# Kernel optimization log

Hardware: AMD Instinct MI355X
Metric: run time of the kernel (lower is better)

## Reference

```python
import jax, jax.numpy as jnp
import numpy as np

DIM = 192
NUM_HEADS = 6
WIN = (8, 8)
N = WIN[0] * WIN[1]  # 64 tokens per window


def _relative_position_index():
    ch = np.arange(WIN[0]); cw = np.arange(WIN[1])
    coords = np.stack(np.meshgrid(ch, cw, indexing='ij'))          # (2, Wh, Ww)
    flat = coords.reshape(2, -1)                                    # (2, N)
    rel = flat[:, :, None] - flat[:, None, :]                       # (2, N, N)
    rel = rel.transpose(1, 2, 0).copy()                             # (N, N, 2)
    rel[..., 0] += WIN[0] - 1
    rel[..., 1] += WIN[1] - 1
    rel[..., 0] *= 2 * WIN[1] - 1
    return jnp.asarray(rel.sum(-1), dtype=jnp.int32)                # (N, N)

RPI = _relative_position_index()


def setup_inputs() -> dict:
    key = jax.random.key(0)
    ks = jax.random.split(key, 20)
    B_, T, M, C = 128, 4, 4, DIM
    nW = 64
    x = jax.random.normal(ks[0], (B_, T, N, C), dtype=jnp.float32)
    x_kv = jax.random.normal(ks[1], (B_, M, N, C), dtype=jnp.float32)
    u = jax.random.uniform(ks[2], (nW, N, N))
    mask = jnp.where(u > 0.9, jnp.float32(-100.0), jnp.float32(0.0))
    s = 0.02
    p = lambda k, shape: jax.random.normal(k, shape, dtype=jnp.float32) * s
    return {
        'x': x, 'x_kv': x_kv, 'mask': mask,
        'rpb_table': p(ks[3], ((2 * WIN[0] - 1) * (2 * WIN[1] - 1), NUM_HEADS)),
        'q_w': p(ks[4], (C, C)), 'q_b': jnp.zeros((C,), jnp.float32),
        'kv_w': p(ks[5], (2 * C, C)), 'kv_b': jnp.zeros((2 * C,), jnp.float32),
        'pos_emb': jax.random.normal(ks[6], (N, C), dtype=jnp.float32) / C ** 0.5,
        'pq_w': p(ks[7], (C, C)), 'pq_b': jnp.zeros((C,), jnp.float32),
        'pk_w': p(ks[8], (C, C)), 'pk_b': jnp.zeros((C,), jnp.float32),
        'pv_w': p(ks[9], (C, C)), 'pv_b': jnp.zeros((C,), jnp.float32),
        'po_w': p(ks[10], (C, C)), 'po_b': jnp.zeros((C,), jnp.float32),
        'proj_w': p(ks[11], (C, C)), 'proj_b': jnp.zeros((C,), jnp.float32),
    }


def reference(x, x_kv, mask, rpb_table, q_w, q_b, kv_w, kv_b, pos_emb,
              pq_w, pq_b, pk_w, pk_b, pv_w, pv_b, po_w, po_b, proj_w, proj_b):
    B_, T, _, C = x.shape
    M = x_kv.shape[1]
    nH = NUM_HEADS
    hd = C // nH
    scale = hd ** -0.5

    # projections -> (B_, T, nH, N, hd) and (B_, M, nH, N, hd)
    q = (x @ q_w.T + q_b).reshape(B_, T, N, nH, hd).transpose(0, 1, 3, 2, 4)
    kv = (x_kv @ kv_w.T + kv_b).reshape(B_, M, N, 2, nH, hd)
    k = kv[:, :, :, 0].transpose(0, 1, 3, 2, 4)
    v = kv[:, :, :, 1].transpose(0, 1, 3, 2, 4)

    # scores: (B_, T, M, nH, N, N)
    attn = jnp.einsum('bthnd,bmhed->btmhne', q * scale, k)

    # relative position bias gather
    rpb = rpb_table[RPI.reshape(-1)].reshape(N, N, nH).transpose(2, 0, 1)
    attn = attn + rpb[None, None, None]

    # shifted-window mask (per window index within B_ = b * nW)
    nW = mask.shape[0]
    b = B_ // nW
    attn = attn.reshape(b, nW, T, M, nH, N, N) + mask[None, :, None, None, None]
    attn = attn.reshape(B_, T, M, nH, N, N)

    attn = jax.nn.softmax(attn, axis=-1)
    out = jnp.einsum('btmhne,bmhed->btmhnd', attn, v)
    # faithful to torch: transpose(1,2) then reshape (B_, T, M, N, C)
    out = jnp.swapaxes(out, 1, 2).reshape(B_, T, M, N, C)
    xp = out.reshape(B_ * T, M, N, C)

    # AttentionPooling1d over the M reference axis
    avg = xp.mean(axis=1, keepdims=True)
    xp = jnp.concatenate([avg, xp], axis=1) + pos_emb[None, None]   # (BT, M+1, N, C)
    BT = xp.shape[0]
    seq = xp.transpose(1, 2, 0, 3).reshape((M + 1) * N, BT, C)      # (m n) b c
    qq = (seq[:N] @ pq_w.T + pq_b).reshape(N, BT, nH, hd)
    kk = (seq @ pk_w.T + pk_b).reshape(-1, BT, nH, hd)
    vv = (seq @ pv_w.T + pv_b).reshape(-1, BT, nH, hd)
    a = jnp.einsum('qbhd,kbhd->bhqk', qq * scale, kk)
    a = jax.nn.softmax(a, axis=-1)
    o = jnp.einsum('bhqk,kbhd->qbhd', a, vv).reshape(N, BT, C)
    o = o @ po_w.T + po_b                                           # (N, BT, C)
    o = o.transpose(1, 0, 2).reshape(B_, T, N, C)

    o = jax.nn.gelu(o, approximate=False)
    return o @ proj_w.T + proj_b
```

## Files before the change

kernel.cpp:

```cpp
#include <hip/hip_runtime.h>
#include <math.h>


typedef float f32x4 __attribute__((ext_vector_type(4)));
typedef short s16x8 __attribute__((ext_vector_type(8)));
typedef unsigned short u16x4 __attribute__((ext_vector_type(4)));
typedef unsigned short u16x8 __attribute__((ext_vector_type(8)));

__device__ __forceinline__ unsigned short f2bf(float f) {
    union { float f; unsigned u; } c; c.f = f;
    return (unsigned short)((c.u + 0x7fffu + ((c.u >> 16) & 1u)) >> 16);
}
__device__ __forceinline__ float bf2f(unsigned short h) {
    union { unsigned u; float f; } c; c.u = ((unsigned)h) << 16;
    return c.f;
}

__global__ void wcvt_kernel(const float* __restrict__ q_w, const float* __restrict__ kv_w,
                            const float* __restrict__ pq_w, const float* __restrict__ pk_w,
                            const float* __restrict__ pv_w, const float* __restrict__ po_w,
                            const float* __restrict__ proj_w, unsigned short* __restrict__ wbf)
{
    int i = blockIdx.x * 256 + threadIdx.x;
    if (i >= 294912) return;
    const float* src; int off;
    if      (i < 36864)  { src = q_w;    off = 0; }
    else if (i < 110592) { src = kv_w;   off = 36864; }
    else if (i < 147456) { src = pq_w;   off = 110592; }
    else if (i < 184320) { src = pk_w;   off = 147456; }
    else if (i < 221184) { src = pv_w;   off = 184320; }
    else if (i < 258048) { src = po_w;   off = 221184; }
    else                 { src = proj_w; off = 258048; }
    wbf[i] = f2bf(src[i - off]);
}

__global__ void prep_kernel(unsigned short* __restrict__ xp, const float* __restrict__ pos,
                            unsigned short* __restrict__ t0b)
{
    int i = blockIdx.x * 256 + threadIdx.x;
    int c8 = (i % 24) * 8;
    int n  = (i / 24) & 63;
    int bt = i / (24 * 64);
    float4 p0 = *reinterpret_cast<const float4*>(&pos[n * 192 + c8]);
    float4 p1 = *reinterpret_cast<const float4*>(&pos[n * 192 + c8 + 4]);
    float pv[8] = {p0.x, p0.y, p0.z, p0.w, p1.x, p1.y, p1.z, p1.w};
    float acc[8] = {0, 0, 0, 0, 0, 0, 0, 0};
    size_t base = (size_t)bt * 49152 + n * 192 + c8;
#pragma unroll
    for (int m = 0; m < 4; m++) {
        u16x8 v = *reinterpret_cast<const u16x8*>(&xp[base + m * 12288]);
        u16x8 o;
#pragma unroll
        for (int e = 0; e < 8; e++) {
            float f = bf2f(v[e]) + pv[e];
            acc[e] += f;
            o[e] = f2bf(f);
        }
        *reinterpret_cast<u16x8*>(&xp[base + m * 12288]) = o;
    }
    u16x8 t;
#pragma unroll
    for (int e = 0; e < 8; e++) t[e] = f2bf(acc[e] * 0.25f);
    *reinterpret_cast<u16x8*>(&t0b[(size_t)(bt * 64 + n) * 192 + c8]) = t;
}

template <int SRC, int EPI, int OUTBF>
__global__ __launch_bounds__(256, 3)
void mgemm_kernel(const float* __restrict__ A, const unsigned short* __restrict__ Ab,
                  const unsigned short* __restrict__ Ab2,
                  const unsigned short* __restrict__ W0, const unsigned short* __restrict__ W1,
                  const float* __restrict__ b0, const float* __restrict__ b1,
                  void* __restrict__ C0v, void* __restrict__ C1v, int c0)
{
    __shared__ __align__(16) char As[128 * 192];
    __shared__ __align__(16) char Bs[96 * 192];
    const int tid = threadIdx.x;
    const int gm0 = blockIdx.x * 128;
    const int gn0 = blockIdx.y * 96;
    const int wid = tid >> 6;
    const int wm = wid >> 1, wn = wid & 1;
    const int lane = tid & 63;
    const int lr = lane & 15;
    const int lk = lane >> 4;

    const bool hiN = (gn0 >= 192);
    const unsigned short* Wsel = (EPI == 3 && hiN) ? W1 : W0;
    const int wrow0 = (EPI == 3 && hiN) ? (gn0 - 192) : gn0;

    f32x4 acc[4][3];
#pragma unroll
    for (int i = 0; i < 4; i++)
#pragma unroll
        for (int j = 0; j < 3; j++) acc[i][j] = (f32x4){0.f, 0.f, 0.f, 0.f};

    for (int kb = 0; kb < 192; kb += 96) {
        if (SRC == 0) {
#pragma unroll
            for (int it = 0; it < 12; it++) {
                int f4 = tid + it * 256;
                int row = f4 / 24;
                int kc4 = (f4 - row * 24) * 4;
                float4 v = *reinterpret_cast<const float4*>(
                    &A[(size_t)(gm0 + row) * 192 + kb + kc4]);
                u16x4 bvv;
                bvv[0] = f2bf(v.x); bvv[1] = f2bf(v.y);
                bvv[2] = f2bf(v.z); bvv[3] = f2bf(v.w);
                int boff = (kc4 * 2) ^ ((row & 3) << 4);
                *reinterpret_cast<u16x4*>(As + row * 192 + boff) = bvv;
            }
        } else {
#pragma unroll
            for (int it = 0; it < 6; it++) {
                int f8 = tid + it * 256;
                int row = f8 / 12;
                int c16 = f8 - row * 12;
                const unsigned short* src;
                if (SRC == 3) {
                    src = &Ab[(size_t)(gm0 + row) * 192 + kb + c16 * 8];
                } else {
                    int g = gm0 + row;
                    int bt = g / 320, tok = g - bt * 320; bt += c0;
                    src = (tok < 64)
                        ? &Ab2[(size_t)(bt * 64 + tok) * 192 + kb + c16 * 8]
                        : &Ab[(size_t)bt * 49152 + ((tok >> 6) - 1) * 12288
                              + (tok & 63) * 192 + kb + c16 * 8];
                }
                u16x8 v = *reinterpret_cast<const u16x8*>(src);
                int boff = (c16 * 16) ^ ((row & 3) << 4);
                *reinterpret_cast<u16x8*>(As + row * 192 + boff) = v;
            }
        }
        for (int f8 = tid; f8 < 1152; f8 += 256) {
            int row = f8 / 12;
            int c16 = f8 - row * 12;
            u16x8 v = *reinterpret_cast<const u16x8*>(
                &Wsel[(size_t)(wrow0 + row) * 192 + kb + c16 * 8]);
            int boff = (c16 * 16) ^ ((row & 3) << 4);
            *reinterpret_cast<u16x8*>(Bs + row * 192 + boff) = v;
        }
        __syncthreads();

#pragma unroll
        for (int ks = 0; ks < 3; ks++) {
            s16x8 af[4], bf[3];
#pragma unroll
            for (int i = 0; i < 4; i++) {
                int row = wm * 64 + i * 16 + lr;
                int off = (ks * 64 + lk * 16) ^ ((row & 3) << 4);
                af[i] = *reinterpret_cast<const s16x8*>(As + row * 192 + off);
            }
#pragma unroll
            for (int j = 0; j < 3; j++) {
                int row = wn * 48 + j * 16 + lr;
                int off = (ks * 64 + lk * 16) ^ ((row & 3) << 4);
                bf[j] = *reinterpret_cast<const s16x8*>(Bs + row * 192 + off);
            }
#pragma unroll
            for (int i = 0; i < 4; i++)
#pragma unroll
                for (int j = 0; j < 3; j++)
                    acc[i][j] = __builtin_amdgcn_mfma_f32_16x16x32_bf16(
                        af[i], bf[j], acc[i][j], 0, 0, 0);
        }
        __syncthreads();
    }

#pragma unroll
    for (int j = 0; j < 3; j++) {
        int bcol = gn0 + wn * 48 + j * 16 + lr;
        float bv = (EPI == 3 && bcol >= 192) ? b1[bcol - 192] : b0[bcol];
        void* dst = C0v;
        int oc = bcol;
        if ((EPI == 2 || EPI == 3) && bcol >= 192) { dst = C1v; oc = bcol - 192; }
#pragma unroll
        for (int i = 0; i < 4; i++) {
            int rbase = gm0 + wm * 64 + i * 16 + lk * 4;
#pragma unroll
            for (int r = 0; r < 4; r++) {
                float v = acc[i][j][r] + bv;
                if (EPI == 1) v = 0.5f * v * (1.f + erff(v * 0.70710678118654752440f));
                size_t idx = (size_t)(rbase + r) * 192 + oc;
                if (OUTBF) ((unsigned short*)dst)[idx] = f2bf(v);
                else       ((float*)dst)[idx] = v;
            }
        }
    }
}

__global__ __launch_bounds__(768, 1)
void winattn_kernel(const float* __restrict__ qbuf,
                    const unsigned short* __restrict__ kbuf,
                    const unsigned short* __restrict__ vbuf,
                    const float* __restrict__ mask,
                    const float* __restrict__ rpbt, unsigned short* __restrict__ xp)
{
    __shared__ float klds[64 * 192];
    __shared__ float vlds[64 * 192];
    __shared__ float mlds[64 * 65];
    __shared__ float rldsT[6 * 225];
    __shared__ float exm[768];
    __shared__ float exl[768];
    __shared__ unsigned obuf[6 * 64 * 17];
    const int tid = threadIdx.x;
    const int bid = blockIdx.x;
    const int bb = bid >> 4;
    const int t = (bid >> 2) & 3;
    const int m = bid & 3;
    const int w = tid >> 6;
    const int h = w >> 1;
    const int lane = tid & 63;

    const int kvbase = (bb * 4 + m) * 12288;
#pragma unroll
    for (int it = 0; it < 2; it++) {
        int i8 = tid + it * 768;
        u16x8 kq = *reinterpret_cast<const u16x8*>(&kbuf[kvbase + i8 * 8]);
        u16x8 vq = *reinterpret_cast<const u16x8*>(&vbuf[kvbase + i8 * 8]);
        f32x4 k0, k1, v0, v1;
#pragma unroll
        for (int e = 0; e < 4; e++) {
            k0[e] = bf2f(kq[e]); k1[e] = bf2f(kq[e + 4]);
            v0[e] = bf2f(vq[e]); v1[e] = bf2f(vq[e + 4]);
        }
        *reinterpret_cast<f32x4*>(&klds[i8 * 8]) = k0;
        *reinterpret_cast<f32x4*>(&klds[i8 * 8 + 4]) = k1;
        *reinterpret_cast<f32x4*>(&vlds[i8 * 8]) = v0;
        *reinterpret_cast<f32x4*>(&vlds[i8 * 8 + 4]) = v1;
    }
    const int widx = bb & 63;
    for (int f = tid; f < 4096; f += 768)
        mlds[(f >> 6) * 65 + (f & 63)] = mask[widx * 4096 + f];
    for (int f = tid; f < 1350; f += 768) {
        int hh = f / 225, rr = f - hh * 225;
        rldsT[f] = rpbt[rr * 6 + hh];
    }

    float qreg[32];
    const int qbase = ((bb * 4 + t) * 64 + lane) * 192 + h * 32;
#pragma unroll
    for (int j = 0; j < 8; j++) {
        float4 v = *reinterpret_cast<const float4*>(&qbuf[qbase + j * 4]);
        qreg[4 * j] = v.x; qreg[4 * j + 1] = v.y;
        qreg[4 * j + 2] = v.z; qreg[4 * j + 3] = v.w;
    }
    __syncthreads();

    const float scale = 0.17677669529663688110f;
    const int ni = lane >> 3, nj = lane & 7;
    const int e0 = (w & 1) << 5;
    float s[32];
#pragma unroll
    for (int ee = 0; ee < 32; ee++) {
        int e = e0 + ee;
        const float4* kr = reinterpret_cast<const float4*>(&klds[e * 192 + h * 32]);
        float d0 = 0, d1 = 0, d2 = 0, d3 = 0;
#pragma unroll
        for (int q8 = 0; q8 < 8; q8++) {
            float4 k4 = kr[q8];
            d0 += qreg[q8 * 4] * k4.x;
            d1 += qreg[q8 * 4 + 1] * k4.y;
            d2 += qreg[q8 * 4 + 2] * k4.z;
            d3 += qreg[q8 * 4 + 3] * k4.w;
        }
        int ridx = (ni - (e >> 3) + 7) * 15 + (nj - (e & 7) + 7);
        s[ee] = (d0 + d1 + d2 + d3) * scale + rldsT[h * 225 + ridx] + mlds[lane * 65 + e];
    }
    float mrun = s[0];
#pragma unroll
    for (int ee = 1; ee < 32; ee++) mrun = fmaxf(mrun, s[ee]);
    float lrun = 0.f;
#pragma unroll
    for (int ee = 0; ee < 32; ee++) { s[ee] = __expf(s[ee] - mrun); lrun += s[ee]; }

    float o[32];
#pragma unroll
    for (int d = 0; d < 32; d++) o[d] = 0.f;
#pragma unroll
    for (int ee = 0; ee < 32; ee++) {
        float p = s[ee];
        const float4* vr = reinterpret_cast<const float4*>(&vlds[(e0 + ee) * 192 + h * 32]);
#pragma unroll
        for (int d8 = 0; d8 < 8; d8++) {
            float4 v4 = vr[d8];
            o[d8 * 4] += p * v4.x; o[d8 * 4 + 1] += p * v4.y;
            o[d8 * 4 + 2] += p * v4.z; o[d8 * 4 + 3] += p * v4.w;
        }
    }

    __syncthreads();
    exm[w * 64 + lane] = mrun;
    __syncthreads();
    float mo = exm[(w ^ 1) * 64 + lane];
    float mt = fmaxf(mrun, mo);
    float fs = __expf(mrun - mt);
    if (w & 1) {
        unsigned* ob = &obuf[h * 1088 + lane * 17];
#pragma unroll
        for (int j = 0; j < 16; j++) {
            unsigned lo = f2bf(fs * o[2 * j]);
            unsigned hi = f2bf(fs * o[2 * j + 1]);
            ob[j] = lo | (hi << 16);
        }
        exl[w * 64 + lane] = fs * lrun;
    }
    __syncthreads();
    if (!(w & 1)) {
        float lt = fs * lrun + exl[(w + 1) * 64 + lane];
        const float inv = 1.f / lt;
        const unsigned* ob = &obuf[h * 1088 + lane * 17];
        const int obase = bb * 196608 + m * 49152 + t * 12288 + h * 2048 + lane * 32;
#pragma unroll
        for (int j = 0; j < 8; j++) {
            unsigned p0 = ob[2 * j], p1 = ob[2 * j + 1];
            u16x4 v;
            v[0] = f2bf((fs * o[4 * j]     + bf2f((unsigned short)(p0 & 0xffff))) * inv);
            v[1] = f2bf((fs * o[4 * j + 1] + bf2f((unsigned short)(p0 >> 16))) * inv);
            v[2] = f2bf((fs * o[4 * j + 2] + bf2f((unsigned short)(p1 & 0xffff))) * inv);
            v[3] = f2bf((fs * o[4 * j + 3] + bf2f((unsigned short)(p1 >> 16))) * inv);
            *reinterpret_cast<u16x4*>(&xp[obase + j * 4]) = v;
        }
    }
}

__global__ __launch_bounds__(320)
void poolattn3_kernel(const unsigned short* __restrict__ kk,
                      const unsigned short* __restrict__ vv,
                      const float* __restrict__ qq,
                      unsigned short* __restrict__ opool, int c0)
{
    __shared__ float ubuf[10560];
    __shared__ float scm[320], scl[320];
    const int tid = threadIdx.x;
    const int w = tid >> 6, lane = tid & 63;
    const int h = blockIdx.x, btl = blockIdx.y;
    const int bt = c0 + btl;
    float* Kf = ubuf + w * 2048;
    float* Vf = Kf + 1024;

    float qreg[32];
    const size_t qbase = (size_t)(bt * 64 + lane) * 192 + h * 32;
#pragma unroll
    for (int j = 0; j < 8; j++) {
        float4 v = *reinterpret_cast<const float4*>(&qq[qbase + j * 4]);
        qreg[4 * j] = v.x; qreg[4 * j + 1] = v.y;
        qreg[4 * j + 2] = v.z; qreg[4 * j + 3] = v.w;
    }
    const float scale = 0.17677669529663688110f;
    float mrun = -3.0e38f, lrun = 0.f;
    float o[32];
#pragma unroll
    for (int d = 0; d < 32; d++) o[d] = 0.f;

#pragma unroll
    for (int it = 0; it < 2; it++) {
        const int tt = w + it * 5;
        const unsigned short* ks = kk + (size_t)(btl * 320 + tt * 32) * 192 + h * 32;
        const unsigned short* vs = vv + (size_t)(btl * 320 + tt * 32) * 192 + h * 32;
#pragma unroll
        for (int ci = 0; ci < 2; ci++) {
            int idx = lane + ci * 64;
            int j = idx >> 2, q4 = (idx & 3) * 8;
            s16x8 kv8 = *reinterpret_cast<const s16x8*>(&ks[j * 192 + q4]);
            s16x8 vv8 = *reinterpret_cast<const s16x8*>(&vs[j * 192 + q4]);
            f32x4 lo, hi, vlo, vhi;
#pragma unroll
            for (int e = 0; e < 4; e++) {
                lo[e] = bf2f((unsigned short)kv8[e]);
                hi[e] = bf2f((unsigned short)kv8[e + 4]);
                vlo[e] = bf2f((unsigned short)vv8[e]);
                vhi[e] = bf2f((unsigned short)vv8[e + 4]);
            }
            *reinterpret_cast<f32x4*>(Kf + j * 32 + q4) = lo;
            *reinterpret_cast<f32x4*>(Kf + j * 32 + q4 + 4) = hi;
            *reinterpret_cast<f32x4*>(Vf + j * 32 + q4) = vlo;
            *reinterpret_cast<f32x4*>(Vf + j * 32 + q4 + 4) = vhi;
        }
        float s[32];
#pragma unroll
        for (int j = 0; j < 32; j++) {
            const float4* kr = reinterpret_cast<const float4*>(Kf + j * 32);
            float d0 = 0, d1 = 0, d2 = 0, d3 = 0;
#pragma unroll
            for (int q8 = 0; q8 < 8; q8++) {
                float4 k4 = kr[q8];
                d0 += qreg[q8 * 4] * k4.x;
                d1 += qreg[q8 * 4 + 1] * k4.y;
                d2 += qreg[q8 * 4 + 2] * k4.z;
                d3 += qreg[q8 * 4 + 3] * k4.w;
            }
            s[j] = (d0 + d1 + d2 + d3) * scale;
        }
        float mt = s[0];
#pragma unroll
        for (int j = 1; j < 32; j++) mt = fmaxf(mt, s[j]);
        float mnew = fmaxf(mrun, mt);
        float fct = __expf(mrun - mnew);
        lrun *= fct;
#pragma unroll
        for (int d = 0; d < 32; d++) o[d] *= fct;
#pragma unroll
        for (int j = 0; j < 32; j++) { float p = __expf(s[j] - mnew); lrun += p; s[j] = p; }
#pragma unroll
        for (int j = 0; j < 32; j++) {
            float p = s[j];
            const float4* vr = reinterpret_cast<const float4*>(Vf + j * 32);
#pragma unroll
            for (int d8 = 0; d8 < 8; d8++) {
                float4 v4 = vr[d8];
                o[d8 * 4] += p * v4.x; o[d8 * 4 + 1] += p * v4.y;
                o[d8 * 4 + 2] += p * v4.z; o[d8 * 4 + 3] += p * v4.w;
            }
        }
        mrun = mnew;
    }
    __syncthreads();
    scm[w * 64 + lane] = mrun;
    scl[w * 64 + lane] = lrun;
#pragma unroll
    for (int d = 0; d < 32; d++) ubuf[w * 2112 + lane * 33 + d] = o[d];
    __syncthreads();

    if (w == 0) {
        float m5 = scm[lane];
#pragma unroll
        for (int ww = 1; ww < 5; ww++) m5 = fmaxf(m5, scm[ww * 64 + lane]);
        float den = 0.f;
        float od[32];
#pragma unroll
        for (int d = 0; d < 32; d++) od[d] = 0.f;
#pragma unroll
        for (int ww = 0; ww < 5; ww++) {
            float f = __expf(scm[ww * 64 + lane] - m5);
            den += f * scl[ww * 64 + lane];
            const float* src = ubuf + ww * 2112 + lane * 33;
#pragma unroll
            for (int d = 0; d < 32; d++) od[d] += f * src[d];
        }
        const float inv = 1.f / den;
        const size_t ob = (size_t)(bt * 64 + lane) * 192 + h * 32;
#pragma unroll
        for (int j = 0; j < 8; j++) {
            u16x4 v;
            v[0] = f2bf(od[4 * j] * inv);     v[1] = f2bf(od[4 * j + 1] * inv);
            v[2] = f2bf(od[4 * j + 2] * inv); v[3] = f2bf(od[4 * j + 3] * inv);
            *reinterpret_cast<u16x4*>(&opool[ob + j * 4]) = v;
        }
    }
}

extern "C" void kernel_launch(void* const* d_in, const int* in_sizes, int n_in,
                              void* d_out, int out_size, void* d_ws, size_t ws_size,
                              hipStream_t stream) {
    (void)in_sizes; (void)n_in; (void)out_size; (void)ws_size;
    const float* x      = (const float*)d_in[0];
    const float* x_kv   = (const float*)d_in[1];
    const float* mask   = (const float*)d_in[2];
    const float* rpbt   = (const float*)d_in[3];
    const float* q_w    = (const float*)d_in[4];
    const float* q_b    = (const float*)d_in[5];
    const float* kv_w   = (const float*)d_in[6];
    const float* kv_b   = (const float*)d_in[7];
    const float* pos    = (const float*)d_in[8];
    const float* pq_w   = (const float*)d_in[9];
    const float* pq_b   = (const float*)d_in[10];
    const float* pk_w   = (const float*)d_in[11];
    const float* pk_b   = (const float*)d_in[12];
    const float* pv_w   = (const float*)d_in[13];
    const float* pv_b   = (const float*)d_in[14];
    const float* po_w   = (const float*)d_in[15];
    const float* po_b   = (const float*)d_in[16];
    const float* proj_w = (const float*)d_in[17];
    const float* proj_b = (const float*)d_in[18];
    float* out = (float*)d_out;
    char* ws = (char*)d_ws;

    float*          qbuf   = (float*)(ws);
    unsigned short* xp     = (unsigned short*)(ws + 25165824u);
    unsigned short* kbuf   = (unsigned short*)(ws + 75497472u);
    unsigned short* vbuf   = (unsigned short*)(ws + 88080384u);
    unsigned short* kkc    = (unsigned short*)(ws + 75497472u);
    unsigned short* vvc    = (unsigned short*)(ws + 106954752u);
    unsigned short* t0b    = (unsigned short*)(ws + 138412032u);
    unsigned short* opoolb = (unsigned short*)(ws + 150994944u);
    unsigned short* opob   = (unsigned short*)(ws + 163577856u);
    unsigned short* wbf    = (unsigned short*)(ws + 176160768u);
    float*          qq     = qbuf;

    dim3 blk(256);
    wcvt_kernel<<<1152, blk, 0, stream>>>(q_w, kv_w, pq_w, pk_w, pv_w, po_w, proj_w, wbf);
    mgemm_kernel<0, 0, 0><<<dim3(256, 2), blk, 0, stream>>>(
        x, nullptr, nullptr, wbf, nullptr, q_b, nullptr, qbuf, nullptr, 0);
    mgemm_kernel<0, 2, 1><<<dim3(256, 4), blk, 0, stream>>>(
        x_kv, nullptr, nullptr, wbf + 36864, nullptr, kv_b, nullptr, kbuf, vbuf, 0);
    winattn_kernel<<<2048, 768, 0, stream>>>(qbuf, kbuf, vbuf, mask, rpbt, xp);
    prep_kernel<<<3072, blk, 0, stream>>>(xp, pos, t0b);
    mgemm_kernel<3, 0, 0><<<dim3(256, 2), blk, 0, stream>>>(
        nullptr, t0b, nullptr, wbf + 110592, nullptr, pq_b, nullptr, qq, nullptr, 0);
    for (int c0 = 0; c0 < 512; c0 += 256) {
        mgemm_kernel<4, 3, 1><<<dim3(640, 4), blk, 0, stream>>>(
            nullptr, xp, t0b, wbf + 147456, wbf + 184320, pk_b, pv_b, kkc, vvc, c0);
        poolattn3_kernel<<<dim3(6, 256), 320, 0, stream>>>(kkc, vvc, qq, opoolb, c0);
    }
    mgemm_kernel<3, 1, 1><<<dim3(256, 2), blk, 0, stream>>>(
        nullptr, opoolb, nullptr, wbf + 221184, nullptr, po_b, nullptr, opob, nullptr, 0);
    mgemm_kernel<3, 0, 0><<<dim3(256, 2), blk, 0, stream>>>(
        nullptr, opob, nullptr, wbf + 258048, nullptr, proj_b, nullptr, out, nullptr, 0);
}
```

Measured before the change: 653.4 us.

## Reuse window K/V across T queries, fuse pos-emb add, coalesce bf16 GEMM stores

The window-attention kernel now loops over the 4 query frames inside one block, so each block converts K/V, the mask and the bias table into LDS once instead of four times; the grid shrinks from 2048 to 512 blocks. The positional-embedding add moves into the attention epilogue, so the prep kernel only reads xp to form the mean and no longer writes it back. The bf16-output GEMM epilogue stages its tile in LDS and writes it out as coalesced 16-byte rows instead of scattered 2-byte stores. The trade-off is less parallelism and longer serial work per attention block, plus an extra barrier in the GEMM epilogue.

```diff
diff --git a/kernel.cpp b/kernel.cpp
--- a/kernel.cpp
+++ b/kernel.cpp
@@ -34,29 +34,20 @@
     wbf[i] = f2bf(src[i - off]);
 }
 
-__global__ void prep_kernel(unsigned short* __restrict__ xp, const float* __restrict__ pos,
+__global__ void prep_kernel(const unsigned short* __restrict__ xp,
                             unsigned short* __restrict__ t0b)
 {
     int i = blockIdx.x * 256 + threadIdx.x;
     int c8 = (i % 24) * 8;
     int n  = (i / 24) & 63;
     int bt = i / (24 * 64);
-    float4 p0 = *reinterpret_cast<const float4*>(&pos[n * 192 + c8]);
-    float4 p1 = *reinterpret_cast<const float4*>(&pos[n * 192 + c8 + 4]);
-    float pv[8] = {p0.x, p0.y, p0.z, p0.w, p1.x, p1.y, p1.z, p1.w};
     float acc[8] = {0, 0, 0, 0, 0, 0, 0, 0};
     size_t base = (size_t)bt * 49152 + n * 192 + c8;
 #pragma unroll
     for (int m = 0; m < 4; m++) {
         u16x8 v = *reinterpret_cast<const u16x8*>(&xp[base + m * 12288]);
-        u16x8 o;
-#pragma unroll
-        for (int e = 0; e < 8; e++) {
-            float f = bf2f(v[e]) + pv[e];
-            acc[e] += f;
-            o[e] = f2bf(f);
-        }
-        *reinterpret_cast<u16x8*>(&xp[base + m * 12288]) = o;
+#pragma unroll
+        for (int e = 0; e < 8; e++) acc[e] += bf2f(v[e]);
     }
     u16x8 t;
 #pragma unroll
@@ -165,24 +156,49 @@
         __syncthreads();
     }
 
-#pragma unroll
-    for (int j = 0; j < 3; j++) {
-        int bcol = gn0 + wn * 48 + j * 16 + lr;
-        float bv = (EPI == 3 && bcol >= 192) ? b1[bcol - 192] : b0[bcol];
-        void* dst = C0v;
-        int oc = bcol;
-        if ((EPI == 2 || EPI == 3) && bcol >= 192) { dst = C1v; oc = bcol - 192; }
-#pragma unroll
-        for (int i = 0; i < 4; i++) {
-            int rbase = gm0 + wm * 64 + i * 16 + lk * 4;
-#pragma unroll
-            for (int r = 0; r < 4; r++) {
-                float v = acc[i][j][r] + bv;
-                if (EPI == 1) v = 0.5f * v * (1.f + erff(v * 0.70710678118654752440f));
-                size_t idx = (size_t)(rbase + r) * 192 + oc;
-                if (OUTBF) ((unsigned short*)dst)[idx] = f2bf(v);
-                else       ((float*)dst)[idx] = v;
-            }
+    if (OUTBF == 0) {
+#pragma unroll
+        for (int j = 0; j < 3; j++) {
+            int bcol = gn0 + wn * 48 + j * 16 + lr;
+            float bv = (EPI == 3 && bcol >= 192) ? b1[bcol - 192] : b0[bcol];
+            float* dst = (float*)C0v;
+            int oc = bcol;
+            if ((EPI == 2 || EPI == 3) && bcol >= 192) { dst = (float*)C1v; oc = bcol - 192; }
+#pragma unroll
+            for (int i = 0; i < 4; i++) {
+                int rbase = gm0 + wm * 64 + i * 16 + lk * 4;
+#pragma unroll
+                for (int r = 0; r < 4; r++) {
+                    float v = acc[i][j][r] + bv;
+                    if (EPI == 1) v = 0.5f * v * (1.f + erff(v * 0.70710678118654752440f));
+                    dst[(size_t)(rbase + r) * 192 + oc] = v;
+                }
+            }
+        }
+    } else {
+        unsigned short* As16 = (unsigned short*)As;
+#pragma unroll
+        for (int j = 0; j < 3; j++) {
+            int bcol = gn0 + wn * 48 + j * 16 + lr;
+            float bv = (EPI == 3 && bcol >= 192) ? b1[bcol - 192] : b0[bcol];
+#pragma unroll
+            for (int i = 0; i < 4; i++)
+#pragma unroll
+                for (int r = 0; r < 4; r++) {
+                    float v = acc[i][j][r] + bv;
+                    if (EPI == 1) v = 0.5f * v * (1.f + erff(v * 0.70710678118654752440f));
+                    As16[(wm * 64 + i * 16 + lk * 4 + r) * 96 + wn * 48 + j * 16 + lr] = f2bf(v);
+                }
+        }
+        __syncthreads();
+        unsigned short* dst = (unsigned short*)((((EPI == 2) || (EPI == 3)) && hiN) ? C1v : C0v);
+        const int oc0 = ((((EPI == 2) || (EPI == 3)) && hiN) ? gn0 - 192 : gn0);
+#pragma unroll
+        for (int it = 0; it < 6; it++) {
+            int f8 = tid + it * 256;
+            int row = f8 / 12, c16 = f8 - row * 12;
+            u16x8 v = *reinterpret_cast<const u16x8*>(&As16[row * 96 + c16 * 8]);
+            *reinterpret_cast<u16x8*>(&dst[(size_t)(gm0 + row) * 192 + oc0 + c16 * 8]) = v;
         }
     }
 }
@@ -192,7 +208,8 @@
                     const unsigned short* __restrict__ kbuf,
                     const unsigned short* __restrict__ vbuf,
                     const float* __restrict__ mask,
-                    const float* __restrict__ rpbt, unsigned short* __restrict__ xp)
+                    const float* __restrict__ rpbt, const float* __restrict__ pos,
+                    unsigned short* __restrict__ xp)
 {
     __shared__ float klds[64 * 192];
     __shared__ float vlds[64 * 192];
@@ -203,8 +220,7 @@
     __shared__ unsigned obuf[6 * 64 * 17];
     const int tid = threadIdx.x;
     const int bid = blockIdx.x;
-    const int bb = bid >> 4;
-    const int t = (bid >> 2) & 3;
+    const int bb = bid >> 2;
     const int m = bid & 3;
     const int w = tid >> 6;
     const int h = w >> 1;
@@ -234,90 +250,93 @@
         int hh = f / 225, rr = f - hh * 225;
         rldsT[f] = rpbt[rr * 6 + hh];
     }
-
-    float qreg[32];
-    const int qbase = ((bb * 4 + t) * 64 + lane) * 192 + h * 32;
-#pragma unroll
-    for (int j = 0; j < 8; j++) {
-        float4 v = *reinterpret_cast<const float4*>(&qbuf[qbase + j * 4]);
-        qreg[4 * j] = v.x; qreg[4 * j + 1] = v.y;
-        qreg[4 * j + 2] = v.z; qreg[4 * j + 3] = v.w;
-    }
     __syncthreads();
 
     const float scale = 0.17677669529663688110f;
     const int ni = lane >> 3, nj = lane & 7;
     const int e0 = (w & 1) << 5;
-    float s[32];
-#pragma unroll
-    for (int ee = 0; ee < 32; ee++) {
-        int e = e0 + ee;
-        const float4* kr = reinterpret_cast<const float4*>(&klds[e * 192 + h * 32]);
-        float d0 = 0, d1 = 0, d2 = 0, d3 = 0;
-#pragma unroll
-        for (int q8 = 0; q8 < 8; q8++) {
-            float4 k4 = kr[q8];
-            d0 += qreg[q8 * 4] * k4.x;
-            d1 += qreg[q8 * 4 + 1] * k4.y;
-            d2 += qreg[q8 * 4 + 2] * k4.z;
-            d3 += qreg[q8 * 4 + 3] * k4.w;
-        }
-        int ridx = (ni - (e >> 3) + 7) * 15 + (nj - (e & 7) + 7);
-        s[ee] = (d0 + d1 + d2 + d3) * scale + rldsT[h * 225 + ridx] + mlds[lane * 65 + e];
-    }
-    float mrun = s[0];
-#pragma unroll
-    for (int ee = 1; ee < 32; ee++) mrun = fmaxf(mrun, s[ee]);
-    float lrun = 0.f;
-#pragma unroll
-    for (int ee = 0; ee < 32; ee++) { s[ee] = __expf(s[ee] - mrun); lrun += s[ee]; }
-
-    float o[32];
-#pragma unroll
-    for (int d = 0; d < 32; d++) o[d] = 0.f;
-#pragma unroll
-    for (int ee = 0; ee < 32; ee++) {
-        float p = s[ee];
-        const float4* vr = reinterpret_cast<const float4*>(&vlds[(e0 + ee) * 192 + h * 32]);
-#pragma unroll
-        for (int d8 = 0; d8 < 8; d8++) {
-            float4 v4 = vr[d8];
-            o[d8 * 4] += p * v4.x; o[d8 * 4 + 1] += p * v4.y;
-            o[d8 * 4 + 2] += p * v4.z; o[d8 * 4 + 3] += p * v4.w;
-        }
-    }
-
-    __syncthreads();
-    exm[w * 64 + lane] = mrun;
-    __syncthreads();
-    float mo = exm[(w ^ 1) * 64 + lane];
-    float mt = fmaxf(mrun, mo);
-    float fs = __expf(mrun - mt);
-    if (w & 1) {
-        unsigned* ob = &obuf[h * 1088 + lane * 17];
-#pragma unroll
-        for (int j = 0; j < 16; j++) {
-            unsigned lo = f2bf(fs * o[2 * j]);
-            unsigned hi = f2bf(fs * o[2 * j + 1]);
-            ob[j] = lo | (hi << 16);
-        }
-        exl[w * 64 + lane] = fs * lrun;
-    }
-    __syncthreads();
-    if (!(w & 1)) {
-        float lt = fs * lrun + exl[(w + 1) * 64 + lane];
-        const float inv = 1.f / lt;
-        const unsigned* ob = &obuf[h * 1088 + lane * 17];
-        const int obase = bb * 196608 + m * 49152 + t * 12288 + h * 2048 + lane * 32;
+
+    for (int t = 0; t < 4; t++) {
+        float qreg[32];
+        const int qbase = ((bb * 4 + t) * 64 + lane) * 192 + h * 32;
 #pragma unroll
         for (int j = 0; j < 8; j++) {
-            unsigned p0 = ob[2 * j], p1 = ob[2 * j + 1];
-            u16x4 v;
-            v[0] = f2bf((fs * o[4 * j]     + bf2f((unsigned short)(p0 & 0xffff))) * inv);
-            v[1] = f2bf((fs * o[4 * j + 1] + bf2f((unsigned short)(p0 >> 16))) * inv);
-            v[2] = f2bf((fs * o[4 * j + 2] + bf2f((unsigned short)(p1 & 0xffff))) * inv);
-            v[3] = f2bf((fs * o[4 * j + 3] + bf2f((unsigned short)(p1 >> 16))) * inv);
-            *reinterpret_cast<u16x4*>(&xp[obase + j * 4]) = v;
+            float4 v = *reinterpret_cast<const float4*>(&qbuf[qbase + j * 4]);
+            qreg[4 * j] = v.x; qreg[4 * j + 1] = v.y;
+            qreg[4 * j + 2] = v.z; qreg[4 * j + 3] = v.w;
+        }
+        float s[32];
+#pragma unroll
+        for (int ee = 0; ee < 32; ee++) {
+            int e = e0 + ee;
+            const float4* kr = reinterpret_cast<const float4*>(&klds[e * 192 + h * 32]);
+            float d0 = 0, d1 = 0, d2 = 0, d3 = 0;
+#pragma unroll
+            for (int q8 = 0; q8 < 8; q8++) {
+                float4 k4 = kr[q8];
+                d0 += qreg[q8 * 4] * k4.x;
+                d1 += qreg[q8 * 4 + 1] * k4.y;
+                d2 += qreg[q8 * 4 + 2] * k4.z;
+                d3 += qreg[q8 * 4 + 3] * k4.w;
+            }
+            int ridx = (ni - (e >> 3) + 7) * 15 + (nj - (e & 7) + 7);
+            s[ee] = (d0 + d1 + d2 + d3) * scale + rldsT[h * 225 + ridx] + mlds[lane * 65 + e];
+        }
+        float mrun = s[0];
+#pragma unroll
+        for (int ee = 1; ee < 32; ee++) mrun = fmaxf(mrun, s[ee]);
+        float lrun = 0.f;
+#pragma unroll
+        for (int ee = 0; ee < 32; ee++) { s[ee] = __expf(s[ee] - mrun); lrun += s[ee]; }
+
+        float o[32];
+#pragma unroll
+        for (int d = 0; d < 32; d++) o[d] = 0.f;
+#pragma unroll
+        for (int ee = 0; ee < 32; ee++) {
+            float p = s[ee];
+            const float4* vr = reinterpret_cast<const float4*>(&vlds[(e0 + ee) * 192 + h * 32]);
+#pragma unroll
+            for (int d8 = 0; d8 < 8; d8++) {
+                float4 v4 = vr[d8];
+                o[d8 * 4] += p * v4.x; o[d8 * 4 + 1] += p * v4.y;
+                o[d8 * 4 + 2] += p * v4.z; o[d8 * 4 + 3] += p * v4.w;
+            }
+        }
+
+        __syncthreads();
+        exm[w * 64 + lane] = mrun;
+        __syncthreads();
+        float mo = exm[(w ^ 1) * 64 + lane];
+        float mt = fmaxf(mrun, mo);
+        float fs = __expf(mrun - mt);
+        if (w & 1) {
+            unsigned* ob = &obuf[h * 1088 + lane * 17];
+#pragma unroll
+            for (int j = 0; j < 16; j++) {
+                unsigned lo = f2bf(fs * o[2 * j]);
+                unsigned hi = f2bf(fs * o[2 * j + 1]);
+                ob[j] = lo | (hi << 16);
+            }
+            exl[w * 64 + lane] = fs * lrun;
+        }
+        __syncthreads();
+        if (!(w & 1)) {
+            float lt = fs * lrun + exl[(w + 1) * 64 + lane];
+            const float inv = 1.f / lt;
+            const unsigned* ob = &obuf[h * 1088 + lane * 17];
+            const int obase = bb * 196608 + m * 49152 + t * 12288 + h * 2048 + lane * 32;
+#pragma unroll
+            for (int j = 0; j < 8; j++) {
+                unsigned p0 = ob[2 * j], p1 = ob[2 * j + 1];
+                float4 pv = *reinterpret_cast<const float4*>(&pos[h * 2048 + lane * 32 + j * 4]);
+                u16x4 v;
+                v[0] = f2bf((fs * o[4 * j]     + bf2f((unsigned short)(p0 & 0xffff))) * inv + pv.x);
+                v[1] = f2bf((fs * o[4 * j + 1] + bf2f((unsigned short)(p0 >> 16))) * inv + pv.y);
+                v[2] = f2bf((fs * o[4 * j + 2] + bf2f((unsigned short)(p1 & 0xffff))) * inv + pv.z);
+                v[3] = f2bf((fs * o[4 * j + 3] + bf2f((unsigned short)(p1 >> 16))) * inv + pv.w);
+                *reinterpret_cast<u16x4*>(&xp[obase + j * 4]) = v;
+            }
         }
     }
 }
@@ -492,8 +511,8 @@
         x, nullptr, nullptr, wbf, nullptr, q_b, nullptr, qbuf, nullptr, 0);
     mgemm_kernel<0, 2, 1><<<dim3(256, 4), blk, 0, stream>>>(
         x_kv, nullptr, nullptr, wbf + 36864, nullptr, kv_b, nullptr, kbuf, vbuf, 0);
-    winattn_kernel<<<2048, 768, 0, stream>>>(qbuf, kbuf, vbuf, mask, rpbt, xp);
-    prep_kernel<<<3072, blk, 0, stream>>>(xp, pos, t0b);
+    winattn_kernel<<<512, 768, 0, stream>>>(qbuf, kbuf, vbuf, mask, rpbt, pos, xp);
+    prep_kernel<<<3072, blk, 0, stream>>>(xp, t0b);
     mgemm_kernel<3, 0, 0><<<dim3(256, 2), blk, 0, stream>>>(
         nullptr, t0b, nullptr, wbf + 110592, nullptr, pq_b, nullptr, qq, nullptr, 0);
     for (int c0 = 0; c0 < 512; c0 += 256) {
```

After: 626.3 us. 1.04x faster.
